# Kernel optimization log

Hardware: AMD Instinct MI355X
Metric: run time of the kernel (lower is better)

The kernel has to match this reference:

```python
import jax, jax.numpy as jnp
import numpy as np

IN_SIZE = 4096
OUT_SIZE = 8192


def setup_inputs() -> dict:
    key = jax.random.key(0)
    ks = jax.random.split(key, 7)
    lim = float(np.sqrt(2.0 / IN_SIZE))
    x = jax.random.normal(ks[0], (IN_SIZE,), dtype=jnp.float32)
    mu = jax.random.uniform(ks[1], (OUT_SIZE, IN_SIZE), minval=-lim, maxval=lim, dtype=jnp.float32)
    rho = jnp.full((OUT_SIZE, IN_SIZE), -5.0, dtype=jnp.float32)
    bias_mu = jnp.zeros((OUT_SIZE,), dtype=jnp.float32)
    bias_rho = jnp.full((OUT_SIZE,), -5.0, dtype=jnp.float32)
    eps_w = jax.random.normal(ks[2], (OUT_SIZE, IN_SIZE), dtype=jnp.float32)
    eps_b = jax.random.normal(ks[3], (OUT_SIZE,), dtype=jnp.float32)
    return {"x": x, "mu": mu, "rho": rho, "bias_mu": bias_mu,
            "bias_rho": bias_rho, "eps_w": eps_w, "eps_b": eps_b}


def reference(x, mu, rho, bias_mu, bias_rho, eps_w, eps_b):
    # Reparameterized weight/bias sample fused into a matvec.
    # w = mu + softplus(rho) * eps_w ; b = bias_mu + softplus(bias_rho) * eps_b
    w = mu + jax.nn.softplus(rho) * eps_w          # (out, in)
    b = bias_mu + jax.nn.softplus(bias_rho) * eps_b  # (out,)
    return w @ x + b                                # (out,)
```

## Files before the change

### kernel.cpp

```cpp
#include <hip/hip_runtime.h>

#define IN_SIZE 4096
#define OUT_SIZE 8192

__device__ __forceinline__ float softplus_fast(float r) {
    float a = __builtin_fabsf(r);
    return fmaxf(r, 0.0f) + __logf(1.0f + __expf(-a));
}

__global__ __launch_bounds__(256) void vlinear_matvec(
    const float* __restrict__ x,
    const float* __restrict__ mu,
    const float* __restrict__ rho,
    const float* __restrict__ bias_mu,
    const float* __restrict__ bias_rho,
    const float* __restrict__ eps_w,
    const float* __restrict__ eps_b,
    float* __restrict__ out)
{
    const int row = blockIdx.x;
    const int tid = threadIdx.x;
    const size_t base = (size_t)row * IN_SIZE;

    const float4* __restrict__ mu4  = (const float4*)(mu    + base);
    const float4* __restrict__ rho4 = (const float4*)(rho   + base);
    const float4* __restrict__ ew4  = (const float4*)(eps_w + base);
    const float4* __restrict__ x4   = (const float4*)x;

    float acc = 0.0f;
    #pragma unroll
    for (int k = 0; k < 4; ++k) {
        const int idx = k * 256 + tid;
        const float4 m = mu4[idx];
        const float4 r = rho4[idx];
        const float4 e = ew4[idx];
        const float4 xv = x4[idx];
        acc += (m.x + softplus_fast(r.x) * e.x) * xv.x;
        acc += (m.y + softplus_fast(r.y) * e.y) * xv.y;
        acc += (m.z + softplus_fast(r.z) * e.z) * xv.z;
        acc += (m.w + softplus_fast(r.w) * e.w) * xv.w;
    }

    #pragma unroll
    for (int off = 32; off > 0; off >>= 1)
        acc += __shfl_down(acc, off, 64);

    __shared__ float s_partial[4];
    const int wave = tid >> 6;
    const int lane = tid & 63;
    if (lane == 0) s_partial[wave] = acc;
    __syncthreads();

    if (tid == 0) {
        float sum = s_partial[0] + s_partial[1] + s_partial[2] + s_partial[3];
        const float b = bias_mu[row] + softplus_fast(bias_rho[row]) * eps_b[row];
        out[row] = sum + b;
    }
}

extern "C" void kernel_launch(void* const* d_in, const int* in_sizes, int n_in,
                              void* d_out, int out_size, void* d_ws, size_t ws_size,
                              hipStream_t stream) {
    const float* x        = (const float*)d_in[0];
    const float* mu       = (const float*)d_in[1];
    const float* rho      = (const float*)d_in[2];
    const float* bias_mu  = (const float*)d_in[3];
    const float* bias_rho = (const float*)d_in[4];
    const float* eps_w    = (const float*)d_in[5];
    const float* eps_b    = (const float*)d_in[6];
    float* out = (float*)d_out;

    vlinear_matvec<<<OUT_SIZE, 256, 0, stream>>>(
        x, mu, rho, bias_mu, bias_rho, eps_w, eps_b, out);
}
```

Before: 356.7 us.

## Split matvec rows across many blocks with atomic accumulation and nontemporal loads

Replaces the one-block-per-row kernel with a flat grid where each thread handles a single float4 and each wave reduces its partial sum, then atomically adds it into the output. A separate small kernel first writes the bias into the output. The weight streams use nontemporal loads so they do not pollute the cache. This trades the per-row block with its shared-memory reduction for many more small blocks, 16 atomics per row, an extra kernel launch, and a summation order that is no longer deterministic.

```diff
diff --git a/kernel.cpp b/kernel.cpp
--- a/kernel.cpp
+++ b/kernel.cpp
@@ -2,59 +2,58 @@
 
 #define IN_SIZE 4096
 #define OUT_SIZE 8192
+#define F4_PER_ROW (IN_SIZE / 4)
+
+typedef float floatx4 __attribute__((ext_vector_type(4)));
 
 __device__ __forceinline__ float softplus_fast(float r) {
     float a = __builtin_fabsf(r);
     return fmaxf(r, 0.0f) + __logf(1.0f + __expf(-a));
 }
 
-__global__ __launch_bounds__(256) void vlinear_matvec(
+__global__ __launch_bounds__(256) void bias_init(
+    const float* __restrict__ bias_mu,
+    const float* __restrict__ bias_rho,
+    const float* __restrict__ eps_b,
+    float* __restrict__ out)
+{
+    const int i = blockIdx.x * 256 + threadIdx.x;
+    out[i] = bias_mu[i] + softplus_fast(bias_rho[i]) * eps_b[i];
+}
+
+__global__ __launch_bounds__(256) void vlinear_split(
     const float* __restrict__ x,
     const float* __restrict__ mu,
     const float* __restrict__ rho,
-    const float* __restrict__ bias_mu,
-    const float* __restrict__ bias_rho,
     const float* __restrict__ eps_w,
-    const float* __restrict__ eps_b,
     float* __restrict__ out)
 {
-    const int row = blockIdx.x;
-    const int tid = threadIdx.x;
-    const size_t base = (size_t)row * IN_SIZE;
+    const int tid  = threadIdx.x;
+    const int flat = blockIdx.x * 256 + tid;
 
-    const float4* __restrict__ mu4  = (const float4*)(mu    + base);
-    const float4* __restrict__ rho4 = (const float4*)(rho   + base);
-    const float4* __restrict__ ew4  = (const float4*)(eps_w + base);
-    const float4* __restrict__ x4   = (const float4*)x;
+    const floatx4* __restrict__ mu4  = (const floatx4*)mu;
+    const floatx4* __restrict__ rho4 = (const floatx4*)rho;
+    const floatx4* __restrict__ ew4  = (const floatx4*)eps_w;
+    const floatx4* __restrict__ x4   = (const floatx4*)x;
 
-    float acc = 0.0f;
-    #pragma unroll
-    for (int k = 0; k < 4; ++k) {
-        const int idx = k * 256 + tid;
-        const float4 m = mu4[idx];
-        const float4 r = rho4[idx];
-        const float4 e = ew4[idx];
-        const float4 xv = x4[idx];
-        acc += (m.x + softplus_fast(r.x) * e.x) * xv.x;
-        acc += (m.y + softplus_fast(r.y) * e.y) * xv.y;
-        acc += (m.z + softplus_fast(r.z) * e.z) * xv.z;
-        acc += (m.w + softplus_fast(r.w) * e.w) * xv.w;
-    }
+    const floatx4 m  = __builtin_nontemporal_load(&mu4[flat]);
+    const floatx4 r  = __builtin_nontemporal_load(&rho4[flat]);
+    const floatx4 e  = __builtin_nontemporal_load(&ew4[flat]);
+    const floatx4 xv = x4[flat & (F4_PER_ROW - 1)];
+
+    float acc;
+    acc  = (m.x + softplus_fast(r.x) * e.x) * xv.x;
+    acc += (m.y + softplus_fast(r.y) * e.y) * xv.y;
+    acc += (m.z + softplus_fast(r.z) * e.z) * xv.z;
+    acc += (m.w + softplus_fast(r.w) * e.w) * xv.w;
 
     #pragma unroll
     for (int off = 32; off > 0; off >>= 1)
         acc += __shfl_down(acc, off, 64);
 
-    __shared__ float s_partial[4];
-    const int wave = tid >> 6;
-    const int lane = tid & 63;
-    if (lane == 0) s_partial[wave] = acc;
-    __syncthreads();
-
-    if (tid == 0) {
-        float sum = s_partial[0] + s_partial[1] + s_partial[2] + s_partial[3];
-        const float b = bias_mu[row] + softplus_fast(bias_rho[row]) * eps_b[row];
-        out[row] = sum + b;
+    if ((tid & 63) == 0) {
+        const int row = flat >> 10;
+        atomicAdd(&out[row], acc);
     }
 }
 
@@ -70,6 +69,8 @@
     const float* eps_b    = (const float*)d_in[6];
     float* out = (float*)d_out;
 
-    vlinear_matvec<<<OUT_SIZE, 256, 0, stream>>>(
-        x, mu, rho, bias_mu, bias_rho, eps_w, eps_b, out);
+    bias_init<<<OUT_SIZE / 256, 256, 0, stream>>>(bias_mu, bias_rho, eps_b, out);
+
+    const int n_blocks = (OUT_SIZE * F4_PER_ROW) / 256;
+    vlinear_split<<<n_blocks, 256, 0, stream>>>(x, mu, rho, eps_w, out);
 }
```

New measurement: 341.5 us. 1.04x faster.
